# Kernel optimization log

Measured on AMD Instinct MI355X. Metric: run time of the kernel, lower is better.

## Reference

```python
import jax, jax.numpy as jnp
import numpy as np

V, E, D, B, C = 100000, 256, 128, 8192, 10  # vocab, embedding_size, context_size, batch, window


def setup_inputs() -> dict:
    key = jax.random.key(0)
    ks = jax.random.split(key, 11)
    s = 0.02
    return {
        "x": jax.random.randint(ks[0], (B,), 0, V),
        "context": jax.random.randint(ks[1], (B, C), 0, V),
        "W_emb": jax.random.normal(ks[2], (V, E), jnp.float32) * s,
        "M_w": jax.random.normal(ks[3], (D, E), jnp.float32) * s,
        "M_b": jnp.zeros((D,), jnp.float32),
        "U_w": jax.random.normal(ks[4], (D, 2 * D), jnp.float32) * s,
        "U_b": jnp.zeros((D,), jnp.float32),
        "W_w": jax.random.normal(ks[5], (D, 2 * D), jnp.float32) * s,
        "W_b": jnp.zeros((D,), jnp.float32),
        "prior_mus": jax.random.normal(ks[6], (V, D), jnp.float32) * s,
        # covariance diagonal must be positive for a valid Gaussian (torch would
        # Cholesky-fail otherwise); sample in [0.1, 1.0)
        "prior_sigmas": jax.random.uniform(ks[7], (V, D), jnp.float32, 0.1, 1.0),
    }


def reference(x, context, W_emb, M_w, M_b, U_w, U_b, W_w, W_b, prior_mus, prior_sigmas):
    emb_x = W_emb[x]                       # [B, E]
    emb_c = W_emb[context]                 # [B, C, E]
    Rw = emb_x @ M_w.T + M_b               # [B, D]  (repeated over C slots below)
    Rc = jnp.einsum('bce,de->bcd', emb_c, M_w) + M_b  # [B, C, D]
    RwC = jnp.broadcast_to(Rw[:, None, :], Rc.shape)   # repeat(len(context), 1)
    h = jax.nn.relu(jnp.concatenate([RwC, Rc], axis=-1)).sum(axis=1)  # [B, 2D]
    mu = h @ U_w.T + U_b                   # posterior mean  [B, D]
    sigma = jax.nn.softplus(h @ W_w.T + W_b)  # posterior cov diag [B, D]
    m0 = prior_mus[x]                      # prior mean      [B, D]
    s0 = prior_sigmas[x]                   # prior cov diag  [B, D]
    # closed-form KL(N(m0, diag(s0)) || N(mu, diag(sigma)))
    d = jnp.float32(D)
    kl = 0.5 * ((s0 / sigma).sum(-1)
                + ((mu - m0) ** 2 / sigma).sum(-1)
                - d
                + jnp.log(sigma).sum(-1) - jnp.log(s0).sum(-1))
    return kl  # [B]
```

## Files before the change

kernel.cpp:

```cpp
#include <hip/hip_runtime.h>
#include <hip/hip_bf16.h>
#include <math.h>


#define CTXN  10
#define DDIM  128
#define WS_M   0
#define WS_UW  32768
#define WS_H   98304

typedef short bf16x8 __attribute__((ext_vector_type(8)));
typedef float f32x4  __attribute__((ext_vector_type(4)));

__device__ __forceinline__ uint2 cvt4(float4 v) {
    union { __hip_bfloat162 h2; unsigned u; } a, b;
    a.h2 = __float22bfloat162_rn(make_float2(v.x, v.y));
    b.h2 = __float22bfloat162_rn(make_float2(v.z, v.w));
    return make_uint2(a.u, b.u);
}

__device__ __forceinline__ float softplusf(float v) {
    return fmaxf(v, 0.0f) + log1pf(expf(-fabsf(v)));
}

__global__ __launch_bounds__(256) void k_cvt(
    const float* __restrict__ M_w, const float* __restrict__ U_w,
    const float* __restrict__ W_w, unsigned short* __restrict__ ws)
{
    int which = blockIdx.x >> 5;
    int i = ((blockIdx.x & 31) << 8) | threadIdx.x;
    const float* src = (which == 0) ? M_w : (which == 1) ? U_w : W_w;
    float4 v = ((const float4*)src)[i];
    *(uint2*)&ws[which * 32768 + i * 4] = cvt4(v);
}

#define BT1   8
#define ROWSP 96
#define LP    72
#define ACH   (ROWSP * LP)

__global__ __launch_bounds__(512, 4) void bsg_h(
    const int* __restrict__ x, const int* __restrict__ ctx,
    const float* __restrict__ W_emb, const float* __restrict__ M_b,
    const unsigned short* __restrict__ wsr, unsigned short* __restrict__ hws)
{
    __shared__ unsigned short A_s[2 * ACH];
    __shared__ int idx_s[ROWSP];

    const int tid  = threadIdx.x;
    const int b0   = blockIdx.x * BT1;
    const int w    = tid >> 6;
    const int lane = tid & 63;
    const int l15  = lane & 15;
    const int lg   = lane >> 4;

    if (tid < ROWSP) {
        int c = tid >> 3, b = b0 + (tid & 7);
        idx_s[tid] = (c >= 11) ? 0 : ((c == 0) ? x[b] : ctx[b * CTXN + (c - 1)]);
    }
    __syncthreads();

    const int r0 = tid >> 4, q0 = tid & 15;
    const int r1 = (tid + 512) >> 4, q1 = q0;
    const int r2 = (tid + 1024) >> 4, q2 = q0;

    float4 rr0[3], rr1[3];
    const float4* We = (const float4*)W_emb;
#define LOADC(dst, ch)                                                          \
    {                                                                           \
        dst[0] = We[(size_t)idx_s[r0] * 64 + (ch) * 16 + q0];                   \
        dst[1] = We[(size_t)idx_s[r1] * 64 + (ch) * 16 + q1];                   \
        dst[2] = We[(size_t)idx_s[r2] * 64 + (ch) * 16 + q2];                   \
    }
#define WRITEC(Ab, src)                                                         \
    {                                                                           \
        *(uint2*)&(Ab)[r0 * LP + 4 * q0] = cvt4(src[0]);                        \
        *(uint2*)&(Ab)[r1 * LP + 4 * q1] = cvt4(src[1]);                        \
        *(uint2*)&(Ab)[r2 * LP + 4 * q2] = cvt4(src[2]);                        \
    }

    LOADC(rr0, 0);
    LOADC(rr1, 1);

    const unsigned short* Mb_bf = wsr + WS_M;
    const int mrow = 16 * w + l15;
    f32x4 acc[6] = {};

#pragma unroll
    for (int ch = 0; ch < 4; ++ch) {
        unsigned short* Ab = A_s + (ch & 1) * ACH;
        if (ch & 1) { WRITEC(Ab, rr1); if (ch < 2) LOADC(rr1, ch + 2); }
        else        { WRITEC(Ab, rr0); if (ch < 2) LOADC(rr0, ch + 2); }
        __syncthreads();
        bf16x8 m0 = *(const bf16x8*)&Mb_bf[mrow * 256 + 64 * ch + 8 * lg];
        bf16x8 m1 = *(const bf16x8*)&Mb_bf[mrow * 256 + 64 * ch + 32 + 8 * lg];
        const unsigned short* Abr = A_s + (ch & 1) * ACH;
#pragma unroll
        for (int mt = 0; mt < 6; ++mt) {
            bf16x8 a0 = *(const bf16x8*)&Abr[(16 * mt + l15) * LP + 8 * lg];
            bf16x8 a1 = *(const bf16x8*)&Abr[(16 * mt + l15) * LP + 32 + 8 * lg];
            acc[mt] = __builtin_amdgcn_mfma_f32_16x16x32_bf16(a0, m0, acc[mt], 0, 0, 0);
            acc[mt] = __builtin_amdgcn_mfma_f32_16x16x32_bf16(a1, m1, acc[mt], 0, 0, 0);
        }
    }
#undef LOADC
#undef WRITEC

    const int dg = 16 * w + l15;
    const float mb = M_b[dg];
    float p1[4] = {0, 0, 0, 0}, p2[4] = {0, 0, 0, 0};
#pragma unroll
    for (int mt = 0; mt < 6; ++mt) {
#pragma unroll
        for (int q = 0; q < 4; ++q) {
            float r = fmaxf(acc[mt][q] + mb, 0.0f);
            if (lg < 2) { if (mt == 0) p1[q] = r; else p2[q] += r; }
            else        { if (mt < 5)  p2[q] += r; }
        }
    }
#pragma unroll
    for (int q = 0; q < 4; ++q) {
        float other = __shfl_xor(p2[q], 32);
        if (lg < 2) {
            int b = 4 * lg + q;
            __hip_bfloat16 t1 = __float2bfloat16(10.0f * p1[q]);
            __hip_bfloat16 t2 = __float2bfloat16(p2[q] + other);
            hws[(size_t)(b0 + b) * 256 + dg]       = *(unsigned short*)&t1;
            hws[(size_t)(b0 + b) * 256 + 128 + dg] = *(unsigned short*)&t2;
        }
    }
}

#define BT2  16
#define HLP  264

__global__ __launch_bounds__(512, 4) void bsg_kl(
    const int* __restrict__ x, const float* __restrict__ U_b,
    const float* __restrict__ W_b, const float* __restrict__ pmu,
    const float* __restrict__ psg, const unsigned short* __restrict__ wsr,
    float* __restrict__ out)
{
    __shared__ unsigned short H_s[BT2 * HLP];
    __shared__ float P_s[BT2 * 8];

    const int tid  = threadIdx.x;
    const int b0   = blockIdx.x * BT2;
    const int w    = tid >> 6;
    const int lane = tid & 63;
    const int l15  = lane & 15;
    const int lg   = lane >> 4;
    const int d    = 16 * w + l15;

    float pm[4], ps[4];
#pragma unroll
    for (int q = 0; q < 4; ++q) {
        int xb = x[b0 + 4 * lg + q];
        pm[q] = pmu[(size_t)xb * DDIM + d];
        ps[q] = psg[(size_t)xb * DDIM + d];
    }

    const unsigned short* hws = wsr + WS_H;
    {
        int r = tid >> 5, q = tid & 31;
        *(uint4*)&H_s[r * HLP + 8 * q] =
            *(const uint4*)&hws[(size_t)(b0 + r) * 256 + 8 * q];
    }
    __syncthreads();

    const unsigned short* UWb = wsr + WS_UW;
    f32x4 acc2[2] = {};
#pragma unroll
    for (int ks = 0; ks < 8; ++ks) {
        bf16x8 hf = *(const bf16x8*)&H_s[l15 * HLP + 32 * ks + 8 * lg];
        bf16x8 bu = *(const bf16x8*)&UWb[d * 256 + 32 * ks + 8 * lg];
        bf16x8 bw = *(const bf16x8*)&UWb[(128 + d) * 256 + 32 * ks + 8 * lg];
        acc2[0] = __builtin_amdgcn_mfma_f32_16x16x32_bf16(hf, bu, acc2[0], 0, 0, 0);
        acc2[1] = __builtin_amdgcn_mfma_f32_16x16x32_bf16(hf, bw, acc2[1], 0, 0, 0);
    }

    const float ub = U_b[d], wb = W_b[d];
#pragma unroll
    for (int q = 0; q < 4; ++q) {
        int rb = 4 * lg + q;
        float mu = acc2[0][q] + ub;
        float sg = softplusf(acc2[1][q] + wb);
        float dm = mu - pm[q];
        float p  = ps[q] / sg + dm * dm / sg + logf(sg) - logf(ps[q]);
        p += __shfl_xor(p, 1);
        p += __shfl_xor(p, 2);
        p += __shfl_xor(p, 4);
        p += __shfl_xor(p, 8);
        if (l15 == 0) P_s[rb * 8 + w] = p;
    }
    __syncthreads();
    if (tid < BT2) {
        float s = 0.0f;
#pragma unroll
        for (int k = 0; k < 8; ++k) s += P_s[tid * 8 + k];
        out[b0 + tid] = 0.5f * (s - (float)DDIM);
    }
}

extern "C" void kernel_launch(void* const* d_in, const int* in_sizes, int n_in,
                              void* d_out, int out_size, void* d_ws, size_t ws_size,
                              hipStream_t stream) {
    const int*   x     = (const int*)  d_in[0];
    const int*   ctx   = (const int*)  d_in[1];
    const float* W_emb = (const float*)d_in[2];
    const float* M_w   = (const float*)d_in[3];
    const float* M_b   = (const float*)d_in[4];
    const float* U_w   = (const float*)d_in[5];
    const float* U_b   = (const float*)d_in[6];
    const float* W_w   = (const float*)d_in[7];
    const float* W_b   = (const float*)d_in[8];
    const float* pmu   = (const float*)d_in[9];
    const float* psg   = (const float*)d_in[10];
    float* out = (float*)d_out;
    unsigned short* ws = (unsigned short*)d_ws;

    k_cvt<<<dim3(96), dim3(256), 0, stream>>>(M_w, U_w, W_w, ws);
    bsg_h<<<dim3(8192 / BT1), dim3(512), 0, stream>>>(x, ctx, W_emb, M_b,
                                                      ws, ws + WS_H);
    bsg_kl<<<dim3(8192 / BT2), dim3(512), 0, stream>>>(x, U_b, W_b, pmu, psg,
                                                       ws, out);
}
```

Baseline: 44.26 us.

## Fuse hidden-state and KL kernels into one 1024-thread block kernel

Merges the embedding-projection kernel and the KL kernel into a single kernel that handles 16 batch rows per 1024-thread block. Sixteen waves split the 11 slot tiles into two groups, combine their partial sums through shared memory, and keep h in LDS instead of writing it to workspace and reading it back. This removes one kernel launch and the global round-trip for h, and takes the prior rows' x indices from shared memory. In exchange, half the waves sit idle during the second GEMM and the KL step, the block needs more shared memory and extra barriers, and occupancy may drop.

```diff
diff --git a/kernel.cpp b/kernel.cpp
--- a/kernel.cpp
+++ b/kernel.cpp
@@ -7,7 +7,13 @@
 #define DDIM  128
 #define WS_M   0
 #define WS_UW  32768
-#define WS_H   98304
+
+#define BT    16
+#define ROWSP 192
+#define LP    72
+#define ACH   (ROWSP * LP)
+#define HLP   264
+#define XLP   132
 
 typedef short bf16x8 __attribute__((ext_vector_type(8)));
 typedef float f32x4  __attribute__((ext_vector_type(4)));
@@ -34,56 +40,57 @@
     *(uint2*)&ws[which * 32768 + i * 4] = cvt4(v);
 }
 
-#define BT1   8
-#define ROWSP 96
-#define LP    72
-#define ACH   (ROWSP * LP)
-
-__global__ __launch_bounds__(512, 4) void bsg_h(
+__global__ __launch_bounds__(1024, 2) void bsg_one(
     const int* __restrict__ x, const int* __restrict__ ctx,
     const float* __restrict__ W_emb, const float* __restrict__ M_b,
-    const unsigned short* __restrict__ wsr, unsigned short* __restrict__ hws)
+    const float* __restrict__ U_b,   const float* __restrict__ W_b,
+    const float* __restrict__ pmu,   const float* __restrict__ psg,
+    const unsigned short* __restrict__ wsr, float* __restrict__ out)
 {
-    __shared__ unsigned short A_s[2 * ACH];
-    __shared__ int idx_s[ROWSP];
+    __shared__ __align__(16) unsigned short A_s[2 * ACH];
+    __shared__ __align__(16) unsigned short H_s[BT * HLP];
+    __shared__ int   idx_s[ROWSP];
+    __shared__ float P_s[BT * 8];
 
     const int tid  = threadIdx.x;
-    const int b0   = blockIdx.x * BT1;
+    const int b0   = blockIdx.x * BT;
     const int w    = tid >> 6;
+    const int n    = w & 7;
+    const int mg   = w >> 3;
     const int lane = tid & 63;
     const int l15  = lane & 15;
     const int lg   = lane >> 4;
 
     if (tid < ROWSP) {
-        int c = tid >> 3, b = b0 + (tid & 7);
+        int c = tid >> 4, b = b0 + (tid & 15);
         idx_s[tid] = (c >= 11) ? 0 : ((c == 0) ? x[b] : ctx[b * CTXN + (c - 1)]);
     }
     __syncthreads();
 
     const int r0 = tid >> 4, q0 = tid & 15;
-    const int r1 = (tid + 512) >> 4, q1 = q0;
-    const int r2 = (tid + 1024) >> 4, q2 = q0;
+    const int r1 = r0 + 64;
+    const int r2 = r0 + 128;
 
     float4 rr0[3], rr1[3];
     const float4* We = (const float4*)W_emb;
 #define LOADC(dst, ch)                                                          \
     {                                                                           \
         dst[0] = We[(size_t)idx_s[r0] * 64 + (ch) * 16 + q0];                   \
-        dst[1] = We[(size_t)idx_s[r1] * 64 + (ch) * 16 + q1];                   \
-        dst[2] = We[(size_t)idx_s[r2] * 64 + (ch) * 16 + q2];                   \
+        dst[1] = We[(size_t)idx_s[r1] * 64 + (ch) * 16 + q0];                   \
+        dst[2] = We[(size_t)idx_s[r2] * 64 + (ch) * 16 + q0];                   \
     }
 #define WRITEC(Ab, src)                                                         \
     {                                                                           \
         *(uint2*)&(Ab)[r0 * LP + 4 * q0] = cvt4(src[0]);                        \
-        *(uint2*)&(Ab)[r1 * LP + 4 * q1] = cvt4(src[1]);                        \
-        *(uint2*)&(Ab)[r2 * LP + 4 * q2] = cvt4(src[2]);                        \
+        *(uint2*)&(Ab)[r1 * LP + 4 * q0] = cvt4(src[1]);                        \
+        *(uint2*)&(Ab)[r2 * LP + 4 * q0] = cvt4(src[2]);                        \
     }
 
     LOADC(rr0, 0);
     LOADC(rr1, 1);
 
     const unsigned short* Mb_bf = wsr + WS_M;
-    const int mrow = 16 * w + l15;
+    const int mrow = 16 * n + l15;
     f32x4 acc[6] = {};
 
 #pragma unroll
@@ -97,103 +104,88 @@
         const unsigned short* Abr = A_s + (ch & 1) * ACH;
 #pragma unroll
         for (int mt = 0; mt < 6; ++mt) {
-            bf16x8 a0 = *(const bf16x8*)&Abr[(16 * mt + l15) * LP + 8 * lg];
-            bf16x8 a1 = *(const bf16x8*)&Abr[(16 * mt + l15) * LP + 32 + 8 * lg];
-            acc[mt] = __builtin_amdgcn_mfma_f32_16x16x32_bf16(a0, m0, acc[mt], 0, 0, 0);
-            acc[mt] = __builtin_amdgcn_mfma_f32_16x16x32_bf16(a1, m1, acc[mt], 0, 0, 0);
+            if (mg == 0 || mt < 5) {
+                int tile = 6 * mg + mt;
+                bf16x8 a0 = *(const bf16x8*)&Abr[(16 * tile + l15) * LP + 8 * lg];
+                bf16x8 a1 = *(const bf16x8*)&Abr[(16 * tile + l15) * LP + 32 + 8 * lg];
+                acc[mt] = __builtin_amdgcn_mfma_f32_16x16x32_bf16(a0, m0, acc[mt], 0, 0, 0);
+                acc[mt] = __builtin_amdgcn_mfma_f32_16x16x32_bf16(a1, m1, acc[mt], 0, 0, 0);
+            }
         }
     }
 #undef LOADC
 #undef WRITEC
 
-    const int dg = 16 * w + l15;
+    const int dg = 16 * n + l15;
     const float mb = M_b[dg];
-    float p1[4] = {0, 0, 0, 0}, p2[4] = {0, 0, 0, 0};
-#pragma unroll
-    for (int mt = 0; mt < 6; ++mt) {
-#pragma unroll
-        for (int q = 0; q < 4; ++q) {
-            float r = fmaxf(acc[mt][q] + mb, 0.0f);
-            if (lg < 2) { if (mt == 0) p1[q] = r; else p2[q] += r; }
-            else        { if (mt < 5)  p2[q] += r; }
-        }
-    }
-#pragma unroll
-    for (int q = 0; q < 4; ++q) {
-        float other = __shfl_xor(p2[q], 32);
-        if (lg < 2) {
+    float* X_s = (float*)A_s;
+
+    if (mg == 1) {
+#pragma unroll
+        for (int q = 0; q < 4; ++q) {
+            float s = 0.0f;
+#pragma unroll
+            for (int mt = 0; mt < 5; ++mt) s += fmaxf(acc[mt][q] + mb, 0.0f);
+            X_s[(4 * lg + q) * XLP + dg] = s;
+        }
+    }
+    __syncthreads();
+
+    if (mg == 0) {
+#pragma unroll
+        for (int q = 0; q < 4; ++q) {
+            float h1 = 10.0f * fmaxf(acc[0][q] + mb, 0.0f);
+            float s  = 0.0f;
+#pragma unroll
+            for (int mt = 1; mt < 6; ++mt) s += fmaxf(acc[mt][q] + mb, 0.0f);
+            s += X_s[(4 * lg + q) * XLP + dg];
             int b = 4 * lg + q;
-            __hip_bfloat16 t1 = __float2bfloat16(10.0f * p1[q]);
-            __hip_bfloat16 t2 = __float2bfloat16(p2[q] + other);
-            hws[(size_t)(b0 + b) * 256 + dg]       = *(unsigned short*)&t1;
-            hws[(size_t)(b0 + b) * 256 + 128 + dg] = *(unsigned short*)&t2;
-        }
-    }
-}
-
-#define BT2  16
-#define HLP  264
-
-__global__ __launch_bounds__(512, 4) void bsg_kl(
-    const int* __restrict__ x, const float* __restrict__ U_b,
-    const float* __restrict__ W_b, const float* __restrict__ pmu,
-    const float* __restrict__ psg, const unsigned short* __restrict__ wsr,
-    float* __restrict__ out)
-{
-    __shared__ unsigned short H_s[BT2 * HLP];
-    __shared__ float P_s[BT2 * 8];
-
-    const int tid  = threadIdx.x;
-    const int b0   = blockIdx.x * BT2;
-    const int w    = tid >> 6;
-    const int lane = tid & 63;
-    const int l15  = lane & 15;
-    const int lg   = lane >> 4;
-    const int d    = 16 * w + l15;
+            __hip_bfloat16 t1 = __float2bfloat16(h1);
+            __hip_bfloat16 t2 = __float2bfloat16(s);
+            H_s[b * HLP + dg]       = *(unsigned short*)&t1;
+            H_s[b * HLP + 128 + dg] = *(unsigned short*)&t2;
+        }
+    }
 
     float pm[4], ps[4];
-#pragma unroll
-    for (int q = 0; q < 4; ++q) {
-        int xb = x[b0 + 4 * lg + q];
-        pm[q] = pmu[(size_t)xb * DDIM + d];
-        ps[q] = psg[(size_t)xb * DDIM + d];
-    }
-
-    const unsigned short* hws = wsr + WS_H;
-    {
-        int r = tid >> 5, q = tid & 31;
-        *(uint4*)&H_s[r * HLP + 8 * q] =
-            *(const uint4*)&hws[(size_t)(b0 + r) * 256 + 8 * q];
-    }
-    __syncthreads();
-
-    const unsigned short* UWb = wsr + WS_UW;
-    f32x4 acc2[2] = {};
-#pragma unroll
-    for (int ks = 0; ks < 8; ++ks) {
-        bf16x8 hf = *(const bf16x8*)&H_s[l15 * HLP + 32 * ks + 8 * lg];
-        bf16x8 bu = *(const bf16x8*)&UWb[d * 256 + 32 * ks + 8 * lg];
-        bf16x8 bw = *(const bf16x8*)&UWb[(128 + d) * 256 + 32 * ks + 8 * lg];
-        acc2[0] = __builtin_amdgcn_mfma_f32_16x16x32_bf16(hf, bu, acc2[0], 0, 0, 0);
-        acc2[1] = __builtin_amdgcn_mfma_f32_16x16x32_bf16(hf, bw, acc2[1], 0, 0, 0);
-    }
-
-    const float ub = U_b[d], wb = W_b[d];
-#pragma unroll
-    for (int q = 0; q < 4; ++q) {
-        int rb = 4 * lg + q;
-        float mu = acc2[0][q] + ub;
-        float sg = softplusf(acc2[1][q] + wb);
-        float dm = mu - pm[q];
-        float p  = ps[q] / sg + dm * dm / sg + logf(sg) - logf(ps[q]);
-        p += __shfl_xor(p, 1);
-        p += __shfl_xor(p, 2);
-        p += __shfl_xor(p, 4);
-        p += __shfl_xor(p, 8);
-        if (l15 == 0) P_s[rb * 8 + w] = p;
-    }
-    __syncthreads();
-    if (tid < BT2) {
+    if (w < 8) {
+#pragma unroll
+        for (int q = 0; q < 4; ++q) {
+            int xb = idx_s[4 * lg + q];
+            pm[q] = pmu[(size_t)xb * DDIM + dg];
+            ps[q] = psg[(size_t)xb * DDIM + dg];
+        }
+    }
+    __syncthreads();
+
+    if (w < 8) {
+        const unsigned short* UWb = wsr + WS_UW;
+        f32x4 acc2[2] = {};
+#pragma unroll
+        for (int ks = 0; ks < 8; ++ks) {
+            bf16x8 hf = *(const bf16x8*)&H_s[l15 * HLP + 32 * ks + 8 * lg];
+            bf16x8 bu = *(const bf16x8*)&UWb[dg * 256 + 32 * ks + 8 * lg];
+            bf16x8 bw = *(const bf16x8*)&UWb[(128 + dg) * 256 + 32 * ks + 8 * lg];
+            acc2[0] = __builtin_amdgcn_mfma_f32_16x16x32_bf16(hf, bu, acc2[0], 0, 0, 0);
+            acc2[1] = __builtin_amdgcn_mfma_f32_16x16x32_bf16(hf, bw, acc2[1], 0, 0, 0);
+        }
+        const float ub = U_b[dg], wb = W_b[dg];
+#pragma unroll
+        for (int q = 0; q < 4; ++q) {
+            int rb = 4 * lg + q;
+            float mu = acc2[0][q] + ub;
+            float sg = softplusf(acc2[1][q] + wb);
+            float dm = mu - pm[q];
+            float p  = ps[q] / sg + dm * dm / sg + logf(sg) - logf(ps[q]);
+            p += __shfl_xor(p, 1);
+            p += __shfl_xor(p, 2);
+            p += __shfl_xor(p, 4);
+            p += __shfl_xor(p, 8);
+            if (l15 == 0) P_s[rb * 8 + w] = p;
+        }
+    }
+    __syncthreads();
+    if (tid < BT) {
         float s = 0.0f;
 #pragma unroll
         for (int k = 0; k < 8; ++k) s += P_s[tid * 8 + k];
@@ -219,8 +211,6 @@
     unsigned short* ws = (unsigned short*)d_ws;
 
     k_cvt<<<dim3(96), dim3(256), 0, stream>>>(M_w, U_w, W_w, ws);
-    bsg_h<<<dim3(8192 / BT1), dim3(512), 0, stream>>>(x, ctx, W_emb, M_b,
-                                                      ws, ws + WS_H);
-    bsg_kl<<<dim3(8192 / BT2), dim3(512), 0, stream>>>(x, U_b, W_b, pmu, psg,
-                                                       ws, out);
-}
+    bsg_one<<<dim3(8192 / BT), dim3(1024), 0, stream>>>(
+        x, ctx, W_emb, M_b, U_b, W_b, pmu, psg, ws, out);
+}
```

Result: slower. 46.43 us (+4.9%).
